# Kernel optimization log

Measured on AMD Instinct MI355X. Metric: run time of the kernel, lower is better.

Reference implementation:

```python
import jax, jax.numpy as jnp
import numpy as np

B = 2
H_GRID, W_GRID, RADIUS = 48, 48, 3
D_MODEL, N_HEADS, D_HEAD = 512, 8, 64
N = H_GRID * W_GRID          # 2304 tokens
WSIZE = (2 * RADIUS + 1) ** 2  # 49 neighbors per token
D_ACT = D_HEAD                # d_head even -> d_act = d_head
SCALE = D_ACT ** -0.5
NEG = -1e9


def _grid_neighbors():
    rr = np.arange(N) // W_GRID
    cc = np.arange(N) % W_GRID
    off = np.arange(-RADIUS, RADIUS + 1)
    dr, dc = np.meshgrid(off, off, indexing='ij')
    dr, dc = dr.ravel(), dc.ravel()
    nr = rr[:, None] + dr[None, :]
    nc = cc[:, None] + dc[None, :]
    valid = (nr >= 0) & (nr < H_GRID) & (nc >= 0) & (nc < W_GRID)
    idx = np.clip(nr, 0, H_GRID - 1) * W_GRID + np.clip(nc, 0, W_GRID - 1)
    pos = np.stack([rr, cc], axis=-1).astype(np.float32)
    return idx.astype(np.int32), valid, pos


def setup_inputs() -> dict:
    key = jax.random.key(0)
    ks = jax.random.split(key, 8)
    idx, valid, pos = _grid_neighbors()
    s = D_MODEL ** -0.5
    return {
        'x': jax.random.normal(ks[0], (B, N, D_MODEL), jnp.float32),
        'positions': jnp.asarray(pos),
        'W_Q': jax.random.normal(ks[1], (D_MODEL, N_HEADS * D_HEAD), jnp.float32) * s,
        'W_K': jax.random.normal(ks[2], (D_MODEL, N_HEADS * D_HEAD), jnp.float32) * s,
        'W_V': jax.random.normal(ks[3], (D_MODEL, N_HEADS * D_HEAD), jnp.float32) * s,
        'W_O': jax.random.normal(ks[4], (N_HEADS * D_HEAD, D_MODEL), jnp.float32) * s,
        # learnable active-subspace basis per head (near-identity init, QR'd in fwd)
        'U': jnp.eye(D_HEAD, D_ACT)[None] + 0.05 * jax.random.normal(ks[5], (N_HEADS, D_HEAD, D_ACT), jnp.float32),
        # per-head rotation generator frequencies: theta = dr . freqs per 2x2 block
        'freqs': 0.5 * jax.random.normal(ks[6], (N_HEADS, 2, D_HEAD // 2), jnp.float32),
        'neighbor_index': jnp.asarray(idx),
        'neighbor_mask': jnp.asarray(valid),
    }


def reference(x, positions, W_Q, W_K, W_V, W_O, U, freqs, neighbor_index, neighbor_mask):
    Bt, Nt, _ = x.shape

    def heads(h):  # (B,N,H*d) -> (B,H,N,d)
        return h.reshape(Bt, Nt, N_HEADS, D_HEAD).transpose(0, 2, 1, 3)

    Q = heads(x @ W_Q)
    K = heads(x @ W_K)
    V = heads(x @ W_V)

    # Active subspace projection Pi_act = U_ortho U_ortho^T, applied as x@U@U^T
    U_ortho = jnp.linalg.qr(U)[0]                       # (H, d, d_act)
    Q = jnp.einsum('bhnd,hde,hfe->bhnf', Q, U_ortho, U_ortho)
    K = jnp.einsum('bhnd,hde,hfe->bhnf', K, U_ortho, U_ortho)

    # per-(i,j) relative rotation: block-diagonal 2x2 rotations with
    # angles theta[h,n,w,p] = (r_j - r_i) . freqs[h,:,p]
    drel = positions[neighbor_index] - positions[:, None, :]   # (N,W,2)
    theta = jnp.einsum('nwc,hcp->hnwp', drel, freqs)           # (H,N,W,d/2)
    cos, sin = jnp.cos(theta), jnp.sin(theta)

    K_loc = K[:, :, neighbor_index]                            # (B,H,N,W,d) gather
    Ke, Ko = K_loc[..., 0::2], K_loc[..., 1::2]
    Kr_e = cos[None] * Ke - sin[None] * Ko
    Kr_o = sin[None] * Ke + cos[None] * Ko
    K_rot = jnp.stack([Kr_e, Kr_o], axis=-1).reshape(K_loc.shape)

    scores = jnp.einsum('bhnd,bhnwd->bhnw', Q, K_rot) * SCALE
    scores = jnp.where(neighbor_mask[None, None], scores, NEG)
    w = jax.nn.softmax(scores, axis=-1)

    V_loc = V[:, :, neighbor_index]                            # (B,H,N,W,d)
    out = jnp.einsum('bhnw,bhnwd->bhnd', w, V_loc)
    out = out.transpose(0, 2, 1, 3).reshape(Bt, Nt, N_HEADS * D_HEAD)
    return out @ W_O
```

## Files before the change

### kernel.cpp

```cpp
#include <hip/hip_runtime.h>
#include <math.h>


#define BB 2
#define HGRID 48
#define WGRID 48
#define NNODE (HGRID*WGRID)
#define RAD 3
#define WSZ 49
#define DMODEL 512
#define NHEAD 8
#define SCALE 0.125f
#define MROWS (BB*NNODE)
#define TPAD 141

typedef _Float16 f16;
typedef __attribute__((ext_vector_type(8))) _Float16 f16x8;
typedef __attribute__((ext_vector_type(2))) _Float16 h2;
typedef __attribute__((ext_vector_type(4))) float f32x4;

typedef union { f16x8 v8; h2 h[4]; } pack8;

#if __has_builtin(__builtin_amdgcn_fdot2)
__device__ __forceinline__ float fdot2(h2 a, h2 b, float c) {
    return __builtin_amdgcn_fdot2(a, b, c, false);
}
#else
__device__ __forceinline__ float fdot2(h2 a, h2 b, float c) {
    return fmaf((float)a.x, (float)b.x, fmaf((float)a.y, (float)b.y, c));
}
#endif

__global__ void convert_all(const float* __restrict__ x,
                            const float* __restrict__ WQ, const float* __restrict__ WK,
                            const float* __restrict__ WV, const float* __restrict__ WO,
                            f16* __restrict__ x2, f16* __restrict__ Wall) {
    int id = blockIdx.x * 256 + threadIdx.x;
    if (id < MROWS * 64) {
        int r = id >> 6, c8 = (id & 63) << 3;
        float4 a = *(const float4*)&x[(size_t)r * 512 + c8];
        float4 b = *(const float4*)&x[(size_t)r * 512 + c8 + 4];
        f16 o[8] = {(f16)a.x, (f16)a.y, (f16)a.z, (f16)a.w,
                    (f16)b.x, (f16)b.y, (f16)b.z, (f16)b.w};
        *(f16x8*)&x2[(size_t)r * 512 + c8] = *(f16x8*)o;
        return;
    }
    id -= MROWS * 64;
    if (id >= 2048 * 64) return;
    int np = id >> 6;
    int kb = (id & 63) << 3;
    const float* S;
    int n;
    if (np < 1536) { int t = np >> 9; n = np & 511; S = (t == 0) ? WQ : (t == 1) ? WK : WV; }
    else           { n = np - 1536;  S = WO; }
    f16 o[8];
#pragma unroll
    for (int i = 0; i < 8; ++i) o[i] = (f16)S[(size_t)(kb + i) * 512 + n];
    *(f16x8*)&Wall[(size_t)np * 512 + kb] = *(f16x8*)o;
}

template<int MODE>
__global__ __launch_bounds__(256)
void mgemm(const f16* __restrict__ A, const f16* __restrict__ Bt,
           f16* __restrict__ Qh, f16* __restrict__ Kh, f16* __restrict__ Vh,
           float* __restrict__ Cf, const float* __restrict__ freqs) {
    __shared__ f16 As[128 * 64];
    __shared__ f16 Bs[128 * 64];

    const int tid = threadIdx.x;
    const int l = tid & 63, wid = tid >> 6;
    const int m0 = blockIdx.y * 128;
    const int n0 = blockIdx.x * 128;
    const int wm = (wid >> 1) * 64, wn = (wid & 1) * 64;
    const int fr = l & 15, fk = l >> 4;
    const int srow = l >> 3, slot = l & 7;

    f32x4 acc[4][4];
#pragma unroll
    for (int m = 0; m < 4; ++m)
#pragma unroll
        for (int n = 0; n < 4; ++n) acc[m][n] = (f32x4){0.f, 0.f, 0.f, 0.f};

    for (int kt = 0; kt < 8; ++kt) {
        const int k0 = kt * 64;
#pragma unroll
        for (int j = 0; j < 4; ++j) {
            const int r = wid * 32 + j * 8 + srow;
            const int cA = (slot ^ (r & 7)) * 8;
            const f16* gA = A + (size_t)(m0 + r) * 512 + k0 + cA;
            __builtin_amdgcn_global_load_lds(
                (const __attribute__((address_space(1))) unsigned int*)gA,
                (__attribute__((address_space(3))) unsigned int*)(As + wid * 2048 + j * 512),
                16, 0, 0);
            const f16* gB = Bt + (size_t)(n0 + r) * 512 + k0 + cA;
            __builtin_amdgcn_global_load_lds(
                (const __attribute__((address_space(1))) unsigned int*)gB,
                (__attribute__((address_space(3))) unsigned int*)(Bs + wid * 2048 + j * 512),
                16, 0, 0);
        }
        asm volatile("s_waitcnt vmcnt(0)" ::: "memory");
        __syncthreads();

        f16x8 af[4][2], bfr[4][2];
#pragma unroll
        for (int m = 0; m < 4; ++m) {
            const int row = wm + m * 16 + fr;
#pragma unroll
            for (int kk = 0; kk < 2; ++kk) {
                const int b = (kk * 64 + fk * 16) ^ ((row & 7) << 4);
                af[m][kk] = *(const f16x8*)((const char*)As + row * 128 + b);
            }
        }
#pragma unroll
        for (int n = 0; n < 4; ++n) {
            const int row = wn + n * 16 + fr;
#pragma unroll
            for (int kk = 0; kk < 2; ++kk) {
                const int b = (kk * 64 + fk * 16) ^ ((row & 7) << 4);
                bfr[n][kk] = *(const f16x8*)((const char*)Bs + row * 128 + b);
            }
        }
#pragma unroll
        for (int kk = 0; kk < 2; ++kk)
#pragma unroll
            for (int m = 0; m < 4; ++m)
#pragma unroll
                for (int n = 0; n < 4; ++n)
                    acc[m][n] = __builtin_amdgcn_mfma_f32_16x16x32_f16(
                        af[m][kk], bfr[n][kk], acc[m][n], 0, 0, 0);
        __syncthreads();
    }

    if (MODE == 0) {
#pragma unroll
        for (int nf = 0; nf < 4; ++nf) {
            const int ccol = n0 + wn + nf * 16 + fr;
            const int t = ccol >> 9;
            const int h = (ccol >> 6) & 7;
            const int d = ccol & 63;
            const int p = d >> 1;
            f16* Cp = (t == 0) ? Qh : (t == 1) ? Kh : Vh;
            const float fR = freqs[h * 64 + p];
            const float fC = freqs[h * 64 + 32 + p];
            const float sgn = (d & 1) ? 1.0f : -1.0f;
#pragma unroll
            for (int mf = 0; mf < 4; ++mf) {
#pragma unroll
                for (int i = 0; i < 4; ++i) {
                    const int grow = m0 + wm + mf * 16 + fk * 4 + i;
                    const int b_ = grow >= NNODE;
                    const int nn = grow - b_ * NNODE;
                    float val = acc[mf][nf][i];
                    float part = __shfl_xor(val, 1);
                    float outv = val;
                    if (t < 2) {
                        float th = (float)(nn / WGRID) * fR + (float)(nn % WGRID) * fC;
                        float sn, cs;
                        __sincosf(th, &sn, &cs);
                        outv = fmaf(sgn * part, sn, val * cs);
                    }
                    Cp[((size_t)((b_ * NHEAD + h) * NNODE + nn)) * 64 + d] = (f16)outv;
                }
            }
        }
    } else {
#pragma unroll
        for (int nf = 0; nf < 4; ++nf) {
            const int ccol = n0 + wn + nf * 16 + fr;
#pragma unroll
            for (int mf = 0; mf < 4; ++mf) {
#pragma unroll
                for (int i = 0; i < 4; ++i) {
                    const int grow = m0 + wm + mf * 16 + fk * 4 + i;
                    Cf[(size_t)grow * 512 + ccol] = acc[mf][nf][i];
                }
            }
        }
    }
}

__global__ __launch_bounds__(256, 5)
void attn5(const f16* __restrict__ Qh, const f16* __restrict__ Kh,
           const f16* __restrict__ Vh, f16* __restrict__ out2) {
    __shared__ h2 T[32 * TPAD];

    const int tid = threadIdx.x;
    const int wid = tid >> 6, lane = tid & 63;
    const int qs = lane >> 3, wg = lane & 7;

    const int bid = blockIdx.x;
    const int t  = bid % 72, bh = bid / 72;
    const int tr = t % 12,   tc = t / 12;
    const int r0 = tr * 4,   c0 = tc * 8;
    const int h  = bh & 7,   b_ = bh >> 3;

    const int lr0 = max(0, r0 - 3), lr1 = min(HGRID - 1, r0 + 6);
    const int lc0 = max(0, c0 - 3), lc1 = min(WGRID - 1, c0 + 10);
    const int NR = lr1 - lr0 + 1, NC = lc1 - lc0 + 1;

    const f16* Kb = Kh + (size_t)bh * NNODE * 64;
    const f16* Vb = Vh + (size_t)bh * NNODE * 64;

    const int rq = r0 + wid, cq = c0 + qs;
    const int nq = rq * WGRID + cq;
    const f16* qrow = Qh + ((size_t)bh * NNODE + nq) * 64;
    h2 q2[32];
#pragma unroll
    for (int j8 = 0; j8 < 8; ++j8) {
        pack8 v;
        v.v8 = *(const f16x8*)&qrow[j8 * 8];
#pragma unroll
        for (int k = 0; k < 4; ++k) q2[j8 * 4 + k] = v.h[k];
    }

    const int cnt = NR * NC * 8;
    for (int i = tid; i < cnt; i += 256) {
        const int row = i >> 3, p4 = i & 7;
        const int glr = row / NC, glc = row - glr * NC;
        const int n = (lr0 + glr) * WGRID + (lc0 + glc);
        pack8 v;
        v.v8 = *(const f16x8*)&Kb[(size_t)n * 64 + p4 * 8];
#pragma unroll
        for (int j = 0; j < 4; ++j) T[(p4 * 4 + j) * TPAD + row] = v.h[j];
    }
    __syncthreads();

    float sc[7], es[7];
    float mx = -1e30f;
#pragma unroll
    for (int k = 0; k < 7; ++k) {
        const int w = wg + 8 * k;
        sc[k] = -1e30f;
        if (w < WSZ) {
            const int dr = w / 7 - RAD, dc = w % 7 - RAD;
            const int nr = rq + dr, nc = cq + dc;
            const bool valid = ((unsigned)nr < (unsigned)HGRID) &&
                               ((unsigned)nc < (unsigned)WGRID);
            const int nrl = min(max(nr, lr0), lr1) - lr0;
            const int ncl = min(max(nc, lc0), lc1) - lc0;
            const int row = nrl * NC + ncl;
            float s = 0.0f;
#pragma unroll
            for (int j = 0; j < 32; ++j) s = fdot2(q2[j], T[j * TPAD + row], s);
            sc[k] = valid ? s * SCALE : -1e9f;
            mx = fmaxf(mx, sc[k]);
        }
    }
#pragma unroll
    for (int o = 1; o < 8; o <<= 1) mx = fmaxf(mx, __shfl_xor(mx, o));
    float sum = 0.0f;
#pragma unroll
    for (int k = 0; k < 7; ++k) {
        const int w = wg + 8 * k;
        es[k] = 0.0f;
        if (w < WSZ) { es[k] = __expf(sc[k] - mx); sum += es[k]; }
    }
#pragma unroll
    for (int o = 1; o < 8; o <<= 1) sum += __shfl_xor(sum, o);
    const float inv = 1.0f / sum;
    float esn[7];
#pragma unroll
    for (int k = 0; k < 7; ++k) esn[k] = es[k] * inv;

    __syncthreads();

    for (int i = tid; i < cnt; i += 256) {
        const int row = i >> 3, p4 = i & 7;
        const int glr = row / NC, glc = row - glr * NC;
        const int n = (lr0 + glr) * WGRID + (lc0 + glc);
        pack8 v;
        v.v8 = *(const f16x8*)&Vb[(size_t)n * 64 + p4 * 8];
#pragma unroll
        for (int j = 0; j < 4; ++j) T[(p4 * 4 + j) * TPAD + row] = v.h[j];
    }
    __syncthreads();

    const int dg = wg;
    float2 acc[4] = {{0, 0}, {0, 0}, {0, 0}, {0, 0}};
#pragma unroll
    for (int w = 0; w < WSZ; ++w) {
        const int dr = w / 7 - RAD, dc = w % 7 - RAD;
        const int nr = rq + dr, nc = cq + dc;
        const int nrl = min(max(nr, lr0), lr1) - lr0;
        const int ncl = min(max(nc, lc0), lc1) - lc0;
        const int row = nrl * NC + ncl;
        const float pw = __shfl(esn[w >> 3], (lane & 0x38) | (w & 7));
#pragma unroll
        for (int j = 0; j < 4; ++j) {
            h2 v2 = T[(dg * 4 + j) * TPAD + row];
            acc[j].x = fmaf(pw, (float)v2.x, acc[j].x);
            acc[j].y = fmaf(pw, (float)v2.y, acc[j].y);
        }
    }

    f16 o[8] = {(f16)acc[0].x, (f16)acc[0].y, (f16)acc[1].x, (f16)acc[1].y,
                (f16)acc[2].x, (f16)acc[2].y, (f16)acc[3].x, (f16)acc[3].y};
    const size_t rowb = (size_t)(b_ * NNODE + nq) * 512 + h * 64 + dg * 8;
    *(f16x8*)&out2[rowb] = *(f16x8*)o;
}

extern "C" void kernel_launch(void* const* d_in, const int* in_sizes, int n_in,
                              void* d_out, int out_size, void* d_ws, size_t ws_size,
                              hipStream_t stream) {
    const float* x     = (const float*)d_in[0];
    const float* WQ    = (const float*)d_in[2];
    const float* WK    = (const float*)d_in[3];
    const float* WV    = (const float*)d_in[4];
    const float* WO    = (const float*)d_in[5];
    const float* freqs = (const float*)d_in[7];

    const size_t HN = (size_t)16 * NNODE * 64;
    f16* Qh   = (f16*)d_ws;
    f16* Kh   = Qh + HN;
    f16* Vh   = Kh + HN;
    f16* x2   = Vh + HN;
    f16* Wall = x2 + (size_t)MROWS * 512;
    f16* Wo2  = Wall + (size_t)1536 * 512;

    convert_all<<<((MROWS + 2048) * 64 + 255) / 256, 256, 0, stream>>>(
        x, WQ, WK, WV, WO, x2, Wall);

    dim3 gqkv(12, 36);
    mgemm<0><<<gqkv, 256, 0, stream>>>(x2, Wall, Qh, Kh, Vh, nullptr, freqs);

    attn5<<<16 * 72, 256, 0, stream>>>(Qh, Kh, Vh, x2);

    dim3 go(4, 36);
    mgemm<1><<<go, 256, 0, stream>>>(x2, Wo2, nullptr, nullptr, nullptr,
                                     (float*)d_out, freqs);
}
```

Baseline: 64.82 us.

## Coalesce weight transpose reads, XCD-swizzle GEMM blocks, prefetch V in attention

The weight-conversion kernel now maps adjacent threads to adjacent output columns, so the strided fp32 weight reads are coalesced across a wavefront. Both GEMMs switch to a 1D grid whose block index is remapped as (bid&7)*cpx + bid>>3, which spreads neighbouring tiles across the 8 XCDs for better L2 locality. The attention kernel issues the V-tile global loads into registers before the K-tile staging and the score computation, so V latency overlaps with that work. The extra registers this needs lower the launch-bounds occupancy hint from 5 to 4 blocks per CU.

```diff
diff --git a/kernel.cpp b/kernel.cpp
--- a/kernel.cpp
+++ b/kernel.cpp
@@ -47,8 +47,8 @@
     }
     id -= MROWS * 64;
     if (id >= 2048 * 64) return;
-    int np = id >> 6;
-    int kb = (id & 63) << 3;
+    const int kb = ((id >> 6) & 63) << 3;
+    const int np = (id & 63) + ((id >> 12) << 6);
     const float* S;
     int n;
     if (np < 1536) { int t = np >> 9; n = np & 511; S = (t == 0) ? WQ : (t == 1) ? WK : WV; }
@@ -69,8 +69,14 @@
 
     const int tid = threadIdx.x;
     const int l = tid & 63, wid = tid >> 6;
-    const int m0 = blockIdx.y * 128;
-    const int n0 = blockIdx.x * 128;
+
+    const int nbx = (MODE == 0) ? 12 : 4;
+    const int cpx = (MODE == 0) ? 54 : 18;
+    const int bid = blockIdx.x;
+    const int swz = (bid & 7) * cpx + (bid >> 3);
+    const int m0 = (swz / nbx) * 128;
+    const int n0 = (swz % nbx) * 128;
+
     const int wm = (wid >> 1) * 64, wn = (wid & 1) * 64;
     const int fr = l & 15, fk = l >> 4;
     const int srow = l >> 3, slot = l & 7;
@@ -179,8 +185,8 @@
     }
 }
 
-__global__ __launch_bounds__(256, 5)
-void attn5(const f16* __restrict__ Qh, const f16* __restrict__ Kh,
+__global__ __launch_bounds__(256, 4)
+void attn7(const f16* __restrict__ Qh, const f16* __restrict__ Kh,
            const f16* __restrict__ Vh, f16* __restrict__ out2) {
     __shared__ h2 T[32 * TPAD];
 
@@ -214,6 +220,19 @@
     }
 
     const int cnt = NR * NC * 8;
+
+    f16x8 vpre[5];
+#pragma unroll
+    for (int s = 0; s < 5; ++s) {
+        const int i = tid + s * 256;
+        if (i < cnt) {
+            const int row = i >> 3, p4 = i & 7;
+            const int glr = row / NC, glc = row - glr * NC;
+            const int n = (lr0 + glr) * WGRID + (lc0 + glc);
+            vpre[s] = *(const f16x8*)&Vb[(size_t)n * 64 + p4 * 8];
+        }
+    }
+
     for (int i = tid; i < cnt; i += 256) {
         const int row = i >> 3, p4 = i & 7;
         const int glr = row / NC, glc = row - glr * NC;
@@ -264,14 +283,15 @@
 
     __syncthreads();
 
-    for (int i = tid; i < cnt; i += 256) {
-        const int row = i >> 3, p4 = i & 7;
-        const int glr = row / NC, glc = row - glr * NC;
-        const int n = (lr0 + glr) * WGRID + (lc0 + glc);
-        pack8 v;
-        v.v8 = *(const f16x8*)&Vb[(size_t)n * 64 + p4 * 8];
-#pragma unroll
-        for (int j = 0; j < 4; ++j) T[(p4 * 4 + j) * TPAD + row] = v.h[j];
+#pragma unroll
+    for (int s = 0; s < 5; ++s) {
+        const int i = tid + s * 256;
+        if (i < cnt) {
+            const int row = i >> 3, p4 = i & 7;
+            pack8 v; v.v8 = vpre[s];
+#pragma unroll
+            for (int j = 0; j < 4; ++j) T[(p4 * 4 + j) * TPAD + row] = v.h[j];
+        }
     }
     __syncthreads();
 
@@ -320,12 +340,10 @@
     convert_all<<<((MROWS + 2048) * 64 + 255) / 256, 256, 0, stream>>>(
         x, WQ, WK, WV, WO, x2, Wall);
 
-    dim3 gqkv(12, 36);
-    mgemm<0><<<gqkv, 256, 0, stream>>>(x2, Wall, Qh, Kh, Vh, nullptr, freqs);
-
-    attn5<<<16 * 72, 256, 0, stream>>>(Qh, Kh, Vh, x2);
-
-    dim3 go(4, 36);
-    mgemm<1><<<go, 256, 0, stream>>>(x2, Wo2, nullptr, nullptr, nullptr,
-                                     (float*)d_out, freqs);
-}
+    mgemm<0><<<432, 256, 0, stream>>>(x2, Wall, Qh, Kh, Vh, nullptr, freqs);
+
+    attn7<<<16 * 72, 256, 0, stream>>>(Qh, Kh, Vh, x2);
+
+    mgemm<1><<<144, 256, 0, stream>>>(x2, Wo2, nullptr, nullptr, nullptr,
+                                      (float*)d_out, freqs);
+}
```

Result: faster. 60.01 us (-7.4%).
